# Kernel tuning notes

Hardware: AMD Instinct MI355X
Metric: run time of the kernel (lower is better)

The kernel has to match this reference:

```python
import jax, jax.numpy as jnp
import numpy as np

N, M, D = 256, 64, 1024


def _l2norm(x, axis=-1, eps=1e-12):
    # tf.math.l2_normalize semantics: x / sqrt(max(sum(x^2), eps))
    sq = jnp.sum(x * x, axis=axis, keepdims=True)
    return x * jax.lax.rsqrt(jnp.maximum(sq, eps))


def setup_inputs() -> dict:
    key = jax.random.key(0)
    k1, = jax.random.split(key, 1)
    inputs = jax.random.normal(k1, (N * M, D), dtype=jnp.float32)
    w = jnp.full((1,), 10.0, dtype=jnp.float32)
    b = jnp.full((1,), -5.0, dtype=jnp.float32)
    return {"inputs": inputs, "w": w, "b": b}


def reference(inputs, w, b):
    emb = inputs.reshape(N, M, D)                       # (N, M, D)
    # speaker centroids (normalized mean over utterances)
    center = _l2norm(jnp.mean(emb, axis=1))             # (N, D)
    # leave-one-out centroid per utterance: sum over M minus self (NOT divided)
    center_except = _l2norm(jnp.sum(emb, axis=1, keepdims=True) - emb)  # (N, M, D)
    # off-diagonal similarities: every utterance vs every speaker centroid
    sim_all = jnp.einsum('jmd,id->jmi', emb, center)    # (N_utt_spk j, M, N_centroid i)
    # diagonal (i == j): utterance vs its own leave-one-out centroid
    diag = jnp.sum(center_except * emb, axis=-1)        # (N, M)
    eye = jnp.eye(N, dtype=bool)[:, None, :]            # (N, 1, N)
    sim = jnp.where(eye, diag[:, :, None], sim_all)     # (N, M, N)
    sim = w * sim + b
    return sim.reshape(N * M, N)
```

## Files before the change

kernel.cpp:

```cpp
#include <hip/hip_runtime.h>

#define NSPK 256
#define MUTT 64
#define DDIM 1024
#define NROW (NSPK * MUTT)

using frag_ab = __attribute__((ext_vector_type(8))) short;
using frag_cd = __attribute__((ext_vector_type(4))) float;

static __device__ __forceinline__ unsigned short f32_to_bf16(float f) {
    unsigned int u = __float_as_uint(f);
    unsigned int r = (u + 0x7FFFu + ((u >> 16) & 1u)) >> 16;
    return (unsigned short)r;
}

__global__ void k_sums(const float* __restrict__ emb, float* __restrict__ Sp) {
    const int j = blockIdx.x;
    const int h = blockIdx.y;
    const int c = threadIdx.x;
    const float* base = emb + ((size_t)j * MUTT + (size_t)h * 32) * DDIM + (size_t)c * 4;
    float4 acc = make_float4(0.f, 0.f, 0.f, 0.f);
    #pragma unroll 8
    for (int m = 0; m < 32; ++m) {
        float4 v = *(const float4*)(base + (size_t)m * DDIM);
        acc.x += v.x; acc.y += v.y; acc.z += v.z; acc.w += v.w;
    }
    float* dst = Sp + ((size_t)h * NSPK + j) * DDIM + (size_t)c * 4;
    *(float4*)dst = acc;
}

__global__ void k_center(const float* __restrict__ Sp, unsigned short* __restrict__ cbf,
                         float* __restrict__ normS2g, float* __restrict__ normSg) {
    const int j = blockIdx.x;
    const int t = threadIdx.x;
    const float* s0 = Sp + (size_t)j * DDIM + (size_t)t * 4;
    const float* s1 = Sp + ((size_t)NSPK + j) * DDIM + (size_t)t * 4;
    float4 a = *(const float4*)s0;
    float4 b = *(const float4*)s1;
    float4 v = make_float4(a.x + b.x, a.y + b.y, a.z + b.z, a.w + b.w);
    float sq = v.x * v.x + v.y * v.y + v.z * v.z + v.w * v.w;
    #pragma unroll
    for (int off = 32; off > 0; off >>= 1) sq += __shfl_down(sq, off, 64);
    __shared__ float ws[4];
    __shared__ float sc_sh;
    const int lane = t & 63, wave = t >> 6;
    if (lane == 0) ws[wave] = sq;
    __syncthreads();
    if (t == 0) {
        float tot = ws[0] + ws[1] + ws[2] + ws[3];
        normS2g[j] = tot;
        normSg[j]  = sqrtf(tot);
        float msq = tot * (1.0f / 4096.0f);
        sc_sh = rsqrtf(fmaxf(msq, 1e-12f)) * (1.0f / 64.0f);
    }
    __syncthreads();
    const float sc = sc_sh;
    unsigned int p0 = (unsigned)f32_to_bf16(v.x * sc) | ((unsigned)f32_to_bf16(v.y * sc) << 16);
    unsigned int p1 = (unsigned)f32_to_bf16(v.z * sc) | ((unsigned)f32_to_bf16(v.w * sc) << 16);
    *(uint2*)(cbf + (size_t)j * DDIM + (size_t)t * 4) = make_uint2(p0, p1);
}

__global__ void __launch_bounds__(256)
k_gemm(const float* __restrict__ emb,
       const unsigned short* __restrict__ cbf,
       const float* __restrict__ normS2g,
       const float* __restrict__ normSg,
       const float* __restrict__ wp, const float* __restrict__ bp,
       float* __restrict__ out) {
    __shared__ unsigned short Asm[32][32];
    __shared__ unsigned short Bsm[256][32];
    __shared__ float qpart[32][8];
    __shared__ float qfin[32];

    const int tid  = threadIdx.x;
    const int lane = tid & 63;
    const int wave = tid >> 6;
    const int row0 = blockIdx.x * 32;
    const int jspk = row0 >> 6;

    frag_cd acc[2][4];
    #pragma unroll
    for (int rr = 0; rr < 2; ++rr)
        #pragma unroll
        for (int cc = 0; cc < 4; ++cc)
            acc[rr][cc] = (frag_cd){0.f, 0.f, 0.f, 0.f};

    const int ar = tid >> 3;
    const int ak = (tid & 7) << 2;
    const float* aptr = emb + (size_t)(row0 + ar) * DDIM + ak;
    float qacc = 0.f;

    const int bi = tid >> 2;
    const int bk = (tid & 3) << 3;

    const int am = lane & 15;
    const int kq = (lane >> 4) << 3;

    for (int k0 = 0; k0 < DDIM; k0 += 32) {
        __syncthreads();
        float4 av = *(const float4*)(aptr + k0);
        qacc += av.x * av.x + av.y * av.y + av.z * av.z + av.w * av.w;
        unsigned int p0 = (unsigned)f32_to_bf16(av.x) | ((unsigned)f32_to_bf16(av.y) << 16);
        unsigned int p1 = (unsigned)f32_to_bf16(av.z) | ((unsigned)f32_to_bf16(av.w) << 16);
        *(uint2*)&Asm[ar][ak] = make_uint2(p0, p1);
        #pragma unroll
        for (int p = 0; p < 4; ++p) {
            int brow = p * 64 + bi;
            uint4 bv = *(const uint4*)(cbf + (size_t)brow * DDIM + k0 + bk);
            *(uint4*)&Bsm[brow][bk] = bv;
        }
        __syncthreads();
        frag_ab afr[2], bfr[4];
        #pragma unroll
        for (int rr = 0; rr < 2; ++rr)
            afr[rr] = *(const frag_ab*)&Asm[rr * 16 + am][kq];
        #pragma unroll
        for (int cc = 0; cc < 4; ++cc)
            bfr[cc] = *(const frag_ab*)&Bsm[wave * 64 + cc * 16 + am][kq];
        #pragma unroll
        for (int rr = 0; rr < 2; ++rr)
            #pragma unroll
            for (int cc = 0; cc < 4; ++cc)
                acc[rr][cc] = __builtin_amdgcn_mfma_f32_16x16x32_bf16(
                    afr[rr], bfr[cc], acc[rr][cc], 0, 0, 0);
    }

    qpart[ar][tid & 7] = qacc;
    __syncthreads();
    if (tid < 32) {
        float s = 0.f;
        #pragma unroll
        for (int u = 0; u < 8; ++u) s += qpart[tid][u];
        qfin[tid] = s;
    }
    __syncthreads();

    const float wv  = wp[0];
    const float bv  = bp[0];
    const float ns2 = normS2g[jspk];
    const float ns  = normSg[jspk];

    #pragma unroll
    for (int rr = 0; rr < 2; ++rr) {
        int rbase = rr * 16 + ((lane >> 4) << 2);
        #pragma unroll
        for (int cc = 0; cc < 4; ++cc) {
            int col = wave * 64 + cc * 16 + (lane & 15);
            frag_cd v = acc[rr][cc];
            #pragma unroll
            for (int r2 = 0; r2 < 4; ++r2) {
                int lrow = rbase + r2;
                float val = v[r2];
                if (col == jspk) {
                    float q  = qfin[lrow];
                    float rd = val * ns;
                    float den2 = ns2 - 2.f * rd + q;
                    val = (rd - q) * rsqrtf(fmaxf(den2, 1e-12f));
                }
                out[(size_t)(row0 + lrow) * NSPK + col] = wv * val + bv;
            }
        }
    }
}

extern "C" void kernel_launch(void* const* d_in, const int* in_sizes, int n_in,
                              void* d_out, int out_size, void* d_ws, size_t ws_size,
                              hipStream_t stream) {
    const float* emb = (const float*)d_in[0];
    const float* w   = (const float*)d_in[1];
    const float* b   = (const float*)d_in[2];
    float* out = (float*)d_out;

    float* Sp = (float*)d_ws;
    unsigned short* cbf = (unsigned short*)(Sp + 2 * NSPK * DDIM);
    float* normS2g = (float*)(cbf + NSPK * DDIM);
    float* normSg  = normS2g + NSPK;

    k_sums<<<dim3(NSPK, 2), 256, 0, stream>>>(emb, Sp);
    k_center<<<NSPK, 256, 0, stream>>>(Sp, cbf, normS2g, normSg);
    k_gemm<<<NROW / 32, 256, 0, stream>>>(emb, cbf, normS2g, normSg, w, b, out);
}
```

Measured before the change: 131.9 us.

## Pre-convert embeddings to bf16 and use double-buffered direct-to-LDS GEMM

A new prep kernel reads the fp32 embeddings once, writing per-speaker partial sums, per-row squared norms and a bf16 copy. A new GEMM kernel tiles 64 rows by 128 centroid columns with BK=64 and double-buffers tiles in LDS. It fills them with global_load_lds using an XOR swizzle to avoid bank conflicts. This removes the in-loop fp32 conversion and the per-block reload of all 256 centroids, but adds a 32 MB bf16 write and read, and only runs when the workspace is large enough.

```diff
diff --git a/kernel.cpp b/kernel.cpp
--- a/kernel.cpp
+++ b/kernel.cpp
@@ -10,9 +10,197 @@
 
 static __device__ __forceinline__ unsigned short f32_to_bf16(float f) {
     unsigned int u = __float_as_uint(f);
-    unsigned int r = (u + 0x7FFFu + ((u >> 16) & 1u)) >> 16;
-    return (unsigned short)r;
-}
+    return (unsigned short)((u + 0x7FFFu + ((u >> 16) & 1u)) >> 16);
+}
+static __device__ __forceinline__ unsigned int pack2(float a, float b) {
+    return (unsigned)f32_to_bf16(a) | ((unsigned)f32_to_bf16(b) << 16);
+}
+static __device__ __forceinline__ void gload16(const void* g, void* l) {
+    __builtin_amdgcn_global_load_lds(
+        (const __attribute__((address_space(1))) unsigned int*)g,
+        (__attribute__((address_space(3))) unsigned int*)l, 16, 0, 0);
+}
+
+
+__global__ void __launch_bounds__(256) k_prep(const float* __restrict__ emb,
+                                              float* __restrict__ Sp,
+                                              unsigned short* __restrict__ ebf,
+                                              float* __restrict__ qg) {
+    const int j = blockIdx.x;
+    const int h = blockIdx.y;
+    const int t = threadIdx.x;
+    const int lane = t & 63, wave = t >> 6;
+    const size_t rowbase = (size_t)j * MUTT + (size_t)h * 16;
+    const float* src = emb + rowbase * DDIM + (size_t)t * 4;
+    unsigned short* edst = ebf + rowbase * DDIM + (size_t)t * 4;
+    __shared__ float qws[16][4];
+    float4 s = make_float4(0.f, 0.f, 0.f, 0.f);
+    #pragma unroll
+    for (int m = 0; m < 16; ++m) {
+        float4 v = *(const float4*)(src + (size_t)m * DDIM);
+        s.x += v.x; s.y += v.y; s.z += v.z; s.w += v.w;
+        float qp = v.x * v.x + v.y * v.y + v.z * v.z + v.w * v.w;
+        #pragma unroll
+        for (int off = 32; off > 0; off >>= 1) qp += __shfl_down(qp, off, 64);
+        if (lane == 0) qws[m][wave] = qp;
+        *(uint2*)(edst + (size_t)m * DDIM) = make_uint2(pack2(v.x, v.y), pack2(v.z, v.w));
+    }
+    __syncthreads();
+    if (t < 16) qg[rowbase + t] = qws[t][0] + qws[t][1] + qws[t][2] + qws[t][3];
+    *(float4*)(Sp + ((size_t)h * NSPK + j) * DDIM + (size_t)t * 4) = s;
+}
+
+template <int P>
+__global__ void k_center(const float* __restrict__ Sp, unsigned short* __restrict__ cbf,
+                         float* __restrict__ normS2g, float* __restrict__ normSg) {
+    const int j = blockIdx.x;
+    const int t = threadIdx.x;
+    float4 v = make_float4(0.f, 0.f, 0.f, 0.f);
+    #pragma unroll
+    for (int p = 0; p < P; ++p) {
+        float4 a = *(const float4*)(Sp + ((size_t)p * NSPK + j) * DDIM + (size_t)t * 4);
+        v.x += a.x; v.y += a.y; v.z += a.z; v.w += a.w;
+    }
+    float sq = v.x * v.x + v.y * v.y + v.z * v.z + v.w * v.w;
+    #pragma unroll
+    for (int off = 32; off > 0; off >>= 1) sq += __shfl_down(sq, off, 64);
+    __shared__ float ws[4];
+    __shared__ float sc_sh;
+    const int lane = t & 63, wave = t >> 6;
+    if (lane == 0) ws[wave] = sq;
+    __syncthreads();
+    if (t == 0) {
+        float tot = ws[0] + ws[1] + ws[2] + ws[3];
+        normS2g[j] = tot;
+        normSg[j]  = sqrtf(tot);
+        float msq = tot * (1.0f / 4096.0f);
+        sc_sh = rsqrtf(fmaxf(msq, 1e-12f)) * (1.0f / 64.0f);
+    }
+    __syncthreads();
+    const float sc = sc_sh;
+    *(uint2*)(cbf + (size_t)j * DDIM + (size_t)t * 4) =
+        make_uint2(pack2(v.x * sc, v.y * sc), pack2(v.z * sc, v.w * sc));
+}
+
+#define RT 64
+#define CT 128
+#define BK 64
+__global__ void __launch_bounds__(256, 2)
+k_gemm2(const unsigned short* __restrict__ ebf, const unsigned short* __restrict__ cbf,
+        const float* __restrict__ qg, const float* __restrict__ n2g,
+        const float* __restrict__ n1g,
+        const float* __restrict__ wp, const float* __restrict__ bp,
+        float* __restrict__ out) {
+    __shared__ unsigned short lds[2][(RT * BK + CT * BK)];
+
+    const int tid = threadIdx.x, lane = tid & 63, wave = tid >> 6;
+    const int rt = blockIdx.x;
+    const int ct = blockIdx.y;
+    const int row0 = rt * RT;
+    const int c0 = ct * CT;
+    const int jspk = rt;
+
+    int aoff[2], boff[4];
+    #pragma unroll
+    for (int i = 0; i < 2; ++i) {
+        int ca = i * 256 + tid;
+        int row = ca >> 3, sw = ca & 7;
+        aoff[i] = row * (DDIM * 2) + ((sw ^ (row & 7)) << 4);
+    }
+    #pragma unroll
+    for (int i = 0; i < 4; ++i) {
+        int cb = i * 256 + tid;
+        int row = cb >> 3, sw = cb & 7;
+        boff[i] = row * (DDIM * 2) + ((sw ^ (row & 7)) << 4);
+    }
+    const int albase = wave * 512;
+    const char* agbase = (const char*)(ebf + (size_t)row0 * DDIM);
+    const char* bgbase = (const char*)(cbf + (size_t)c0 * DDIM);
+
+    const int quad = lane >> 4;
+    const int m16 = lane & 15;
+    const int wrow = wave >> 1, wcol = wave & 1;
+    int arow[2], brow[4];
+    arow[0] = wrow * 32 + m16; arow[1] = arow[0] + 16;
+    #pragma unroll
+    for (int cc = 0; cc < 4; ++cc) brow[cc] = wcol * 64 + cc * 16 + m16;
+
+    frag_cd acc[2][4];
+    #pragma unroll
+    for (int rr = 0; rr < 2; ++rr)
+        #pragma unroll
+        for (int cc = 0; cc < 4; ++cc) acc[rr][cc] = (frag_cd){0.f, 0.f, 0.f, 0.f};
+
+    #pragma unroll
+    for (int i = 0; i < 2; ++i) gload16(agbase + aoff[i], &lds[0][i * 2048 + albase]);
+    #pragma unroll
+    for (int i = 0; i < 4; ++i) gload16(bgbase + boff[i], &lds[0][4096 + i * 2048 + albase]);
+    __syncthreads();
+
+    const int NIT = DDIM / BK;
+    for (int it = 0; it < NIT; ++it) {
+        const int cur = it & 1;
+        if (it + 1 < NIT) {
+            const char* ag = agbase + (size_t)(it + 1) * BK * 2;
+            const char* bg = bgbase + (size_t)(it + 1) * BK * 2;
+            unsigned short* Ln = &lds[cur ^ 1][0];
+            #pragma unroll
+            for (int i = 0; i < 2; ++i) gload16(ag + aoff[i], Ln + i * 2048 + albase);
+            #pragma unroll
+            for (int i = 0; i < 4; ++i) gload16(bg + boff[i], Ln + 4096 + i * 2048 + albase);
+        }
+        const unsigned short* L = &lds[cur][0];
+        frag_ab af[2][2], bf[4][2];
+        #pragma unroll
+        for (int rr = 0; rr < 2; ++rr)
+            #pragma unroll
+            for (int s = 0; s < 2; ++s) {
+                int addr = arow[rr] * 128 + ((((s << 2) + quad) ^ (arow[rr] & 7)) << 4);
+                af[rr][s] = *(const frag_ab*)&L[addr >> 1];
+            }
+        #pragma unroll
+        for (int cc = 0; cc < 4; ++cc)
+            #pragma unroll
+            for (int s = 0; s < 2; ++s) {
+                int addr = 8192 + brow[cc] * 128 + ((((s << 2) + quad) ^ (brow[cc] & 7)) << 4);
+                bf[cc][s] = *(const frag_ab*)&L[addr >> 1];
+            }
+        #pragma unroll
+        for (int s = 0; s < 2; ++s)
+            #pragma unroll
+            for (int rr = 0; rr < 2; ++rr)
+                #pragma unroll
+                for (int cc = 0; cc < 4; ++cc)
+                    acc[rr][cc] = __builtin_amdgcn_mfma_f32_16x16x32_bf16(
+                        af[rr][s], bf[cc][s], acc[rr][cc], 0, 0, 0);
+        __syncthreads();
+    }
+
+    const float wv = wp[0], bv = bp[0];
+    const float ns2 = n2g[jspk], ns = n1g[jspk];
+    #pragma unroll
+    for (int rr = 0; rr < 2; ++rr) {
+        int rbase = wrow * 32 + rr * 16 + (quad << 2);
+        #pragma unroll
+        for (int cc = 0; cc < 4; ++cc) {
+            int col = c0 + wcol * 64 + cc * 16 + m16;
+            frag_cd v = acc[rr][cc];
+            #pragma unroll
+            for (int r2 = 0; r2 < 4; ++r2) {
+                int grow = row0 + rbase + r2;
+                float val = v[r2];
+                if (col == jspk) {
+                    float q = qg[grow];
+                    float rd = val * ns;
+                    float den2 = ns2 - 2.f * rd + q;
+                    val = (rd - q) * rsqrtf(fmaxf(den2, 1e-12f));
+                }
+                out[(size_t)grow * NSPK + col] = wv * val + bv;
+            }
+        }
+    }
+}
+
 
 __global__ void k_sums(const float* __restrict__ emb, float* __restrict__ Sp) {
     const int j = blockIdx.x;
@@ -25,106 +213,53 @@
         float4 v = *(const float4*)(base + (size_t)m * DDIM);
         acc.x += v.x; acc.y += v.y; acc.z += v.z; acc.w += v.w;
     }
-    float* dst = Sp + ((size_t)h * NSPK + j) * DDIM + (size_t)c * 4;
-    *(float4*)dst = acc;
-}
-
-__global__ void k_center(const float* __restrict__ Sp, unsigned short* __restrict__ cbf,
-                         float* __restrict__ normS2g, float* __restrict__ normSg) {
-    const int j = blockIdx.x;
-    const int t = threadIdx.x;
-    const float* s0 = Sp + (size_t)j * DDIM + (size_t)t * 4;
-    const float* s1 = Sp + ((size_t)NSPK + j) * DDIM + (size_t)t * 4;
-    float4 a = *(const float4*)s0;
-    float4 b = *(const float4*)s1;
-    float4 v = make_float4(a.x + b.x, a.y + b.y, a.z + b.z, a.w + b.w);
-    float sq = v.x * v.x + v.y * v.y + v.z * v.z + v.w * v.w;
-    #pragma unroll
-    for (int off = 32; off > 0; off >>= 1) sq += __shfl_down(sq, off, 64);
-    __shared__ float ws[4];
-    __shared__ float sc_sh;
-    const int lane = t & 63, wave = t >> 6;
-    if (lane == 0) ws[wave] = sq;
-    __syncthreads();
-    if (t == 0) {
-        float tot = ws[0] + ws[1] + ws[2] + ws[3];
-        normS2g[j] = tot;
-        normSg[j]  = sqrtf(tot);
-        float msq = tot * (1.0f / 4096.0f);
-        sc_sh = rsqrtf(fmaxf(msq, 1e-12f)) * (1.0f / 64.0f);
-    }
-    __syncthreads();
-    const float sc = sc_sh;
-    unsigned int p0 = (unsigned)f32_to_bf16(v.x * sc) | ((unsigned)f32_to_bf16(v.y * sc) << 16);
-    unsigned int p1 = (unsigned)f32_to_bf16(v.z * sc) | ((unsigned)f32_to_bf16(v.w * sc) << 16);
-    *(uint2*)(cbf + (size_t)j * DDIM + (size_t)t * 4) = make_uint2(p0, p1);
+    *(float4*)(Sp + ((size_t)h * NSPK + j) * DDIM + (size_t)c * 4) = acc;
 }
 
 __global__ void __launch_bounds__(256)
-k_gemm(const float* __restrict__ emb,
-       const unsigned short* __restrict__ cbf,
-       const float* __restrict__ normS2g,
-       const float* __restrict__ normSg,
-       const float* __restrict__ wp, const float* __restrict__ bp,
-       float* __restrict__ out) {
+k_gemm_old(const float* __restrict__ emb, const unsigned short* __restrict__ cbf,
+           const float* __restrict__ normS2g, const float* __restrict__ normSg,
+           const float* __restrict__ wp, const float* __restrict__ bp,
+           float* __restrict__ out) {
     __shared__ unsigned short Asm[32][32];
     __shared__ unsigned short Bsm[256][32];
     __shared__ float qpart[32][8];
     __shared__ float qfin[32];
-
-    const int tid  = threadIdx.x;
-    const int lane = tid & 63;
-    const int wave = tid >> 6;
+    const int tid = threadIdx.x, lane = tid & 63, wave = tid >> 6;
     const int row0 = blockIdx.x * 32;
     const int jspk = row0 >> 6;
-
     frag_cd acc[2][4];
     #pragma unroll
     for (int rr = 0; rr < 2; ++rr)
         #pragma unroll
-        for (int cc = 0; cc < 4; ++cc)
-            acc[rr][cc] = (frag_cd){0.f, 0.f, 0.f, 0.f};
-
-    const int ar = tid >> 3;
-    const int ak = (tid & 7) << 2;
+        for (int cc = 0; cc < 4; ++cc) acc[rr][cc] = (frag_cd){0.f, 0.f, 0.f, 0.f};
+    const int ar = tid >> 3, ak = (tid & 7) << 2;
     const float* aptr = emb + (size_t)(row0 + ar) * DDIM + ak;
     float qacc = 0.f;
-
-    const int bi = tid >> 2;
-    const int bk = (tid & 3) << 3;
-
-    const int am = lane & 15;
-    const int kq = (lane >> 4) << 3;
-
+    const int bi = tid >> 2, bk = (tid & 3) << 3;
+    const int am = lane & 15, kq = (lane >> 4) << 3;
     for (int k0 = 0; k0 < DDIM; k0 += 32) {
         __syncthreads();
         float4 av = *(const float4*)(aptr + k0);
         qacc += av.x * av.x + av.y * av.y + av.z * av.z + av.w * av.w;
-        unsigned int p0 = (unsigned)f32_to_bf16(av.x) | ((unsigned)f32_to_bf16(av.y) << 16);
-        unsigned int p1 = (unsigned)f32_to_bf16(av.z) | ((unsigned)f32_to_bf16(av.w) << 16);
-        *(uint2*)&Asm[ar][ak] = make_uint2(p0, p1);
+        *(uint2*)&Asm[ar][ak] = make_uint2(pack2(av.x, av.y), pack2(av.z, av.w));
         #pragma unroll
         for (int p = 0; p < 4; ++p) {
             int brow = p * 64 + bi;
-            uint4 bv = *(const uint4*)(cbf + (size_t)brow * DDIM + k0 + bk);
-            *(uint4*)&Bsm[brow][bk] = bv;
+            *(uint4*)&Bsm[brow][bk] = *(const uint4*)(cbf + (size_t)brow * DDIM + k0 + bk);
         }
         __syncthreads();
         frag_ab afr[2], bfr[4];
         #pragma unroll
+        for (int rr = 0; rr < 2; ++rr) afr[rr] = *(const frag_ab*)&Asm[rr * 16 + am][kq];
+        #pragma unroll
+        for (int cc = 0; cc < 4; ++cc) bfr[cc] = *(const frag_ab*)&Bsm[wave * 64 + cc * 16 + am][kq];
+        #pragma unroll
         for (int rr = 0; rr < 2; ++rr)
-            afr[rr] = *(const frag_ab*)&Asm[rr * 16 + am][kq];
-        #pragma unroll
-        for (int cc = 0; cc < 4; ++cc)
-            bfr[cc] = *(const frag_ab*)&Bsm[wave * 64 + cc * 16 + am][kq];
-        #pragma unroll
-        for (int rr = 0; rr < 2; ++rr)
             #pragma unroll
             for (int cc = 0; cc < 4; ++cc)
-                acc[rr][cc] = __builtin_amdgcn_mfma_f32_16x16x32_bf16(
-                    afr[rr], bfr[cc], acc[rr][cc], 0, 0, 0);
-    }
-
+                acc[rr][cc] = __builtin_amdgcn_mfma_f32_16x16x32_bf16(afr[rr], bfr[cc], acc[rr][cc], 0, 0, 0);
+    }
     qpart[ar][tid & 7] = qacc;
     __syncthreads();
     if (tid < 32) {
@@ -134,12 +269,8 @@
         qfin[tid] = s;
     }
     __syncthreads();
-
-    const float wv  = wp[0];
-    const float bv  = bp[0];
-    const float ns2 = normS2g[jspk];
-    const float ns  = normSg[jspk];
-
+    const float wv = wp[0], bv = bp[0];
+    const float ns2 = normS2g[jspk], ns = normSg[jspk];
     #pragma unroll
     for (int rr = 0; rr < 2; ++rr) {
         int rbase = rr * 16 + ((lane >> 4) << 2);
@@ -152,7 +283,7 @@
                 int lrow = rbase + r2;
                 float val = v[r2];
                 if (col == jspk) {
-                    float q  = qfin[lrow];
+                    float q = qfin[lrow];
                     float rd = val * ns;
                     float den2 = ns2 - 2.f * rd + q;
                     val = (rd - q) * rsqrtf(fmaxf(den2, 1e-12f));
@@ -171,12 +302,30 @@
     const float* b   = (const float*)d_in[2];
     float* out = (float*)d_out;
 
-    float* Sp = (float*)d_ws;
-    unsigned short* cbf = (unsigned short*)(Sp + 2 * NSPK * DDIM);
-    float* normS2g = (float*)(cbf + NSPK * DDIM);
-    float* normSg  = normS2g + NSPK;
-
-    k_sums<<<dim3(NSPK, 2), 256, 0, stream>>>(emb, Sp);
-    k_center<<<NSPK, 256, 0, stream>>>(Sp, cbf, normS2g, normSg);
-    k_gemm<<<NROW / 32, 256, 0, stream>>>(emb, cbf, normS2g, normSg, w, b, out);
-}
+    const size_t sz_Sp  = (size_t)4 * NSPK * DDIM * 4;
+    const size_t sz_ebf = (size_t)NROW * DDIM * 2;
+    const size_t sz_cbf = (size_t)NSPK * DDIM * 2;
+    const size_t sz_qg  = (size_t)NROW * 4;
+    const size_t need = sz_Sp + sz_ebf + sz_cbf + sz_qg + 2 * NSPK * 4;
+
+    if (ws_size >= need) {
+        char* p = (char*)d_ws;
+        float* Sp = (float*)p;              p += sz_Sp;
+        unsigned short* ebf = (unsigned short*)p; p += sz_ebf;
+        unsigned short* cbf = (unsigned short*)p; p += sz_cbf;
+        float* qg = (float*)p;              p += sz_qg;
+        float* n2 = (float*)p;              p += NSPK * 4;
+        float* n1 = (float*)p;
+        k_prep<<<dim3(NSPK, 4), 256, 0, stream>>>(emb, Sp, ebf, qg);
+        k_center<4><<<NSPK, 256, 0, stream>>>(Sp, cbf, n2, n1);
+        k_gemm2<<<dim3(NROW / RT, NSPK / CT), 256, 0, stream>>>(ebf, cbf, qg, n2, n1, w, b, out);
+    } else {
+        float* Sp = (float*)d_ws;
+        unsigned short* cbf = (unsigned short*)(Sp + 2 * NSPK * DDIM);
+        float* n2 = (float*)(cbf + NSPK * DDIM);
+        float* n1 = n2 + NSPK;
+        k_sums<<<dim3(NSPK, 2), 256, 0, stream>>>(emb, Sp);
+        k_center<2><<<NSPK, 256, 0, stream>>>(Sp, cbf, n2, n1);
+        k_gemm_old<<<NROW / 32, 256, 0, stream>>>(emb, cbf, n2, n1, w, b, out);
+    }
+}
```

After: 127.2 us. 1.04x faster.
